# Kernel optimization log

Hardware: AMD Instinct MI355X
Metric: run time of the kernel (lower is better)

## Reference

```python
import jax, jax.numpy as jnp
import numpy as np

DIM = 2048
HID = 5632  # multiple_of*ceil((2/3*8192)/256)
CONV = 4
SEQ = 8192


def setup_inputs() -> dict:
    key = jax.random.key(0)
    ks = jax.random.split(key, 6)
    x = jax.random.normal(ks[0], (1, SEQ, DIM), dtype=jnp.float32)
    cu_seqlens = jnp.array([0, 2048, 4096, 6144, 8192], dtype=jnp.int32)
    s = DIM ** -0.5
    w_w = jax.random.normal(ks[1], (HID, DIM), dtype=jnp.float32) * s
    wz_w = jax.random.normal(ks[2], (HID, DIM), dtype=jnp.float32) * s
    wh_w = jax.random.normal(ks[3], (HID, DIM), dtype=jnp.float32) * s
    wo_w = jax.random.normal(ks[4], (DIM, HID), dtype=jnp.float32) * (HID ** -0.5)
    conv_w = jax.random.normal(ks[5], (HID, CONV), dtype=jnp.float32) * (CONV ** -0.5)
    return {"x": x, "cu_seqlens": cu_seqlens, "w_w": w_w, "wz_w": wz_w,
            "wh_w": wh_w, "wo_w": wo_w, "conv_w": conv_w}


def _segment_ids(cu_seqlens, seq_len):
    start = jnp.zeros((seq_len,), dtype=jnp.int32).at[cu_seqlens[:-1]].set(1)
    return start, jnp.cumsum(start)  # start marker, segment id per position


def _causal_conv(z, conv_w, seg_id):
    # z: (b, s, H); depthwise causal conv, w[:, -1] multiplies current step,
    # masked so taps never cross cu_seqlens boundaries.
    s = z.shape[1]
    out = z * conv_w[:, CONV - 1][None, None, :]
    for k in range(1, CONV):
        zs = jnp.pad(z, ((0, 0), (k, 0), (0, 0)))[:, :s]
        sid = jnp.pad(seg_id, (k, 0))[:s]
        valid = (sid == seg_id) & (jnp.arange(s) >= k)
        out = out + zs * conv_w[:, CONV - 1 - k][None, None, :] * valid[None, :, None].astype(z.dtype)
    return out


def _linear_scan(a, b):
    # h_t = a_t * h_{t-1} + b_t along axis=1, via parallel associative scan
    def combine(l, r):
        al, bl = l
        ar, br = r
        return ar * al, ar * bl + br
    _, h = jax.lax.associative_scan(combine, (a, b), axis=1)
    return h


def reference(x, cu_seqlens, w_w, wz_w, wh_w, wo_w, conv_w):
    bsz, seq_len, _ = x.shape
    w0 = jnp.einsum('bsd,hd->bsh', x, w_w)
    z = jnp.einsum('bsd,hd->bsh', x, wz_w)
    tilde_h = jnp.einsum('bsd,hd->bsh', x, wh_w)
    start, seg_id = _segment_ids(cu_seqlens, seq_len)
    z = jax.nn.sigmoid(_causal_conv(z, conv_w, seg_id))
    a = (1.0 - z) * (1 - start)[None, :, None].astype(z.dtype)  # reset state at seq starts
    b = z * tilde_h
    h = _linear_scan(a, b)
    h = h * jax.nn.silu(w0)
    return jnp.einsum('bsh,dh->bsd', h, wo_w)
```

## Files before the change

### kernel.cpp

```cpp
#include <hip/hip_runtime.h>
#include <stdint.h>

#define DIM 2048
#define HID 5632
#define SEQ 8192
#define NW3 (3*HID)
#define CONV 4
#define CHUNK 64

typedef __attribute__((ext_vector_type(8))) __bf16 bf16x8;
typedef __attribute__((ext_vector_type(4))) float f32x4;
typedef __attribute__((ext_vector_type(4))) uint16_t u16x4;

__device__ __forceinline__ uint16_t f2bf(float f) {
  union { float f; uint32_t u; } v; v.f = f;
  return (uint16_t)((v.u + 0x7FFFu + ((v.u >> 16) & 1u)) >> 16);
}
__device__ __forceinline__ float bf2f(uint16_t h) {
  union { uint32_t u; float f; } v; v.u = ((uint32_t)h) << 16;
  return v.f;
}

__global__ void cvt4_kernel(const float* __restrict__ src, uint16_t* __restrict__ dst, int n4) {
  int i = blockIdx.x * blockDim.x + threadIdx.x;
  if (i >= n4) return;
  float4 v = ((const float4*)src)[i];
  ushort4 o;
  o.x = f2bf(v.x); o.y = f2bf(v.y); o.z = f2bf(v.z); o.w = f2bf(v.w);
  ((ushort4*)dst)[i] = o;
}

__device__ __forceinline__ void load_lds16(const void* g, void* l) {
  __builtin_amdgcn_global_load_lds(
      (__attribute__((address_space(1))) void*)g,
      (__attribute__((address_space(3))) void*)l, 16, 0, 0);
}

template<int LDA, int LDB, int LDC, int KLEN, int OUT_MODE>
__global__ __launch_bounds__(512, 2)
void gemm256(const uint16_t* __restrict__ A, const uint16_t* __restrict__ B,
             void* __restrict__ C, int nbx)
{
  __shared__ alignas(16) uint16_t As[2][2][256][32];
  __shared__ alignas(16) uint16_t Bs[2][2][256][32];
  constexpr int NT = KLEN / 64;

  const int tid  = threadIdx.x;
  const int wave = tid >> 6;
  const int lane = tid & 63;

  const int nwg = (int)gridDim.x;
  const int bid = (int)blockIdx.x;
  const int qq  = nwg >> 3, rr = nwg & 7;
  const int xcd = bid & 7, loc = bid >> 3;
  const int swz = (xcd < rr ? xcd*(qq+1) : rr*(qq+1) + (xcd-rr)*qq) + loc;
  const int row0 = (swz % nbx) * 256;
  const int col0 = (swz / nbx) * 256;

  const uint16_t* Ab = A + (size_t)blockIdx.y * KLEN;
  const uint16_t* Bb = B + (size_t)blockIdx.y * KLEN;

  const int wr = wave >> 2;
  const int wc = wave & 3;
  const int rm = lane & 15;
  const int kq8 = ((lane >> 4) ^ ((rm >> 1) & 3)) * 8;
  const int ri = wr*128 + rm;
  const int ci = wc*64 + rm;

  size_t offA0, offA1, offB0, offB1;
  {
    const int g0 = tid,       r0_ = g0 >> 2, k0_ = (g0 & 3) ^ ((r0_ >> 1) & 3);
    const int g1 = 512 + tid, r1_ = g1 >> 2, k1_ = (g1 & 3) ^ ((r1_ >> 1) & 3);
    offA0 = (size_t)(row0 + r0_)*LDA + k0_*8;
    offA1 = (size_t)(row0 + r1_)*LDA + k1_*8;
    offB0 = (size_t)(col0 + r0_)*LDB + k0_*8;
    offB1 = (size_t)(col0 + r1_)*LDB + k1_*8;
  }

#define STAGE_A(kt,h,buf) do {                                              \
    const size_t ko_ = (size_t)(kt)*64 + (size_t)(h)*32;                    \
    load_lds16(Ab + offA0 + ko_, &As[(buf)][(h)][wave*16][0]);              \
    load_lds16(Ab + offA1 + ko_, &As[(buf)][(h)][128 + wave*16][0]);        \
  } while (0)
#define STAGE_B(kt,h,buf) do {                                              \
    const size_t ko_ = (size_t)(kt)*64 + (size_t)(h)*32;                    \
    load_lds16(Bb + offB0 + ko_, &Bs[(buf)][(h)][wave*16][0]);              \
    load_lds16(Bb + offB1 + ko_, &Bs[(buf)][(h)][128 + wave*16][0]);        \
  } while (0)
#define PIN() __builtin_amdgcn_sched_barrier(0)

  f32x4 acc[8][4];
  #pragma unroll
  for (int i = 0; i < 8; ++i)
    #pragma unroll
    for (int j = 0; j < 4; ++j) acc[i][j] = (f32x4){0.f,0.f,0.f,0.f};

  STAGE_A(0,0,0); STAGE_B(0,0,0);
  STAGE_A(0,1,0); STAGE_B(0,1,0);
  {
    const int t1 = (NT > 1) ? 1 : 0;
    STAGE_A(t1,0,1); STAGE_B(t1,0,1);
  }
  asm volatile("s_waitcnt vmcnt(8)" ::: "memory");
  __builtin_amdgcn_s_barrier();
  PIN();

  #pragma unroll 1
  for (int t = 0; t < NT; ++t) {
    const int c   = t & 1;
    const int tn1 = (t+1 < NT) ? t+1 : NT-1;
    const int tn2 = (t+2 < NT) ? t+2 : NT-1;
    bf16x8 af[4], bfr[4];

    #pragma unroll
    for (int i = 0; i < 4; ++i) af[i]  = *(const bf16x8*)&As[c][0][ri + i*16][kq8];
    #pragma unroll
    for (int j = 0; j < 4; ++j) bfr[j] = *(const bf16x8*)&Bs[c][0][ci + j*16][kq8];
    STAGE_A(tn1, 1, c^1);
    PIN();
    __builtin_amdgcn_s_barrier();
    asm volatile("s_waitcnt lgkmcnt(0)" ::: "memory");
    PIN();
    __builtin_amdgcn_s_setprio(1);
    #pragma unroll
    for (int i = 0; i < 4; ++i)
      #pragma unroll
      for (int j = 0; j < 4; ++j)
        acc[i][j] = __builtin_amdgcn_mfma_f32_16x16x32_bf16(af[i], bfr[j], acc[i][j], 0, 0, 0);
    __builtin_amdgcn_s_setprio(0);
    __builtin_amdgcn_s_barrier();
    PIN();

    #pragma unroll
    for (int i = 0; i < 4; ++i) af[i] = *(const bf16x8*)&As[c][0][ri + (i+4)*16][kq8];
    STAGE_B(tn1, 1, c^1);
    PIN();
    __builtin_amdgcn_s_barrier();
    asm volatile("s_waitcnt lgkmcnt(0)" ::: "memory");
    PIN();
    __builtin_amdgcn_s_setprio(1);
    #pragma unroll
    for (int i = 0; i < 4; ++i)
      #pragma unroll
      for (int j = 0; j < 4; ++j)
        acc[i+4][j] = __builtin_amdgcn_mfma_f32_16x16x32_bf16(af[i], bfr[j], acc[i+4][j], 0, 0, 0);
    __builtin_amdgcn_s_setprio(0);
    asm volatile("s_waitcnt vmcnt(8)" ::: "memory");
    __builtin_amdgcn_s_barrier();
    PIN();

    #pragma unroll
    for (int i = 0; i < 4; ++i) af[i]  = *(const bf16x8*)&As[c][1][ri + i*16][kq8];
    #pragma unroll
    for (int j = 0; j < 4; ++j) bfr[j] = *(const bf16x8*)&Bs[c][1][ci + j*16][kq8];
    STAGE_A(tn2, 0, c);
    PIN();
    __builtin_amdgcn_s_barrier();
    asm volatile("s_waitcnt lgkmcnt(0)" ::: "memory");
    PIN();
    __builtin_amdgcn_s_setprio(1);
    #pragma unroll
    for (int i = 0; i < 4; ++i)
      #pragma unroll
      for (int j = 0; j < 4; ++j)
        acc[i][j] = __builtin_amdgcn_mfma_f32_16x16x32_bf16(af[i], bfr[j], acc[i][j], 0, 0, 0);
    __builtin_amdgcn_s_setprio(0);
    __builtin_amdgcn_s_barrier();
    PIN();

    #pragma unroll
    for (int i = 0; i < 4; ++i) af[i] = *(const bf16x8*)&As[c][1][ri + (i+4)*16][kq8];
    STAGE_B(tn2, 0, c);
    PIN();
    __builtin_amdgcn_s_barrier();
    asm volatile("s_waitcnt lgkmcnt(0)" ::: "memory");
    PIN();
    __builtin_amdgcn_s_setprio(1);
    #pragma unroll
    for (int i = 0; i < 4; ++i)
      #pragma unroll
      for (int j = 0; j < 4; ++j)
        acc[i+4][j] = __builtin_amdgcn_mfma_f32_16x16x32_bf16(af[i], bfr[j], acc[i+4][j], 0, 0, 0);
    __builtin_amdgcn_s_setprio(0);
    asm volatile("s_waitcnt vmcnt(8)" ::: "memory");
    __builtin_amdgcn_s_barrier();
    PIN();
  }
#undef STAGE_A
#undef STAGE_B
#undef PIN

  const int cr = (lane >> 4) * 4;
  const int cc = lane & 15;
  #pragma unroll
  for (int i = 0; i < 8; ++i)
    #pragma unroll
    for (int j = 0; j < 4; ++j) {
      const int r_ = row0 + wr*128 + i*16 + cr;
      const int c_ = col0 + wc*64  + j*16 + cc;
      #pragma unroll
      for (int r = 0; r < 4; ++r) {
        const float v = acc[i][j][r];
        const size_t idx = (size_t)(r_ + r)*LDC + c_;
        if (OUT_MODE == 1)      ((uint16_t*)C)[idx] = f2bf(v);
        else if (OUT_MODE == 2) atomicAdd((float*)C + idx, v);
        else                    ((float*)C)[idx] = v;
      }
    }
}


__device__ __forceinline__ void seg_info(const int* cuv, int ns, int t, int& ss, bool& st) {
  ss = 0; st = false;
  for (int i=0;i<ns;i++) { int cv = cuv[i]; if (cv<=t && cv>ss) ss=cv; if (cv==t) st=true; }
}

__global__ void scan_chunk(const uint16_t* __restrict__ G, int qstart,
                           const uint16_t* __restrict__ zprev,
                           const float* __restrict__ convw,
                           const int* __restrict__ cu, int ncu,
                           float* __restrict__ Ach, float* __restrict__ Bch)
{
  const int h0 = (blockIdx.x * blockDim.x + threadIdx.x) * 4;
  const int c  = blockIdx.y;
  const uint16_t* Z  = G + HID;
  const uint16_t* TH = G + 2*HID;
  float4 wv[4];
  #pragma unroll
  for (int j=0;j<4;j++) wv[j] = ((const float4*)convw)[h0+j];
  int cuv[8];
  int ns = ncu - 1; if (ns > 8) ns = 8;
  for (int i=0;i<ns;i++) cuv[i] = cu[i];
  const int r0 = c * CHUNK;
  const int t0 = qstart + r0;
  float z1[4], z2[4], z3[4];
  if (c == 0) {
    u16x4 a1 = *(const u16x4*)&zprev[2*HID + h0];
    u16x4 a2 = *(const u16x4*)&zprev[1*HID + h0];
    u16x4 a3 = *(const u16x4*)&zprev[0*HID + h0];
    #pragma unroll
    for (int j=0;j<4;j++) {
      z1[j] = (t0-1 >= 0) ? bf2f(a1[j]) : 0.f;
      z2[j] = (t0-2 >= 0) ? bf2f(a2[j]) : 0.f;
      z3[j] = (t0-3 >= 0) ? bf2f(a3[j]) : 0.f;
    }
  } else {
    u16x4 a1 = *(const u16x4*)&Z[(size_t)(r0-1)*NW3 + h0];
    u16x4 a2 = *(const u16x4*)&Z[(size_t)(r0-2)*NW3 + h0];
    u16x4 a3 = *(const u16x4*)&Z[(size_t)(r0-3)*NW3 + h0];
    #pragma unroll
    for (int j=0;j<4;j++) { z1[j]=bf2f(a1[j]); z2[j]=bf2f(a2[j]); z3[j]=bf2f(a3[j]); }
  }
  float Aacc[4] = {1.f,1.f,1.f,1.f};
  float Bacc[4] = {0.f,0.f,0.f,0.f};
  u16x4 zv = *(const u16x4*)&Z[(size_t)r0*NW3 + h0];
  u16x4 tv = *(const u16x4*)&TH[(size_t)r0*NW3 + h0];
  for (int r = r0; r < r0 + CHUNK; ++r) {
    const int rn = (r+1 < r0+CHUNK) ? r+1 : r;
    u16x4 zn = *(const u16x4*)&Z[(size_t)rn*NW3 + h0];
    u16x4 tn = *(const u16x4*)&TH[(size_t)rn*NW3 + h0];
    const int t = qstart + r;
    int ss; bool st;
    seg_info(cuv, ns, t, ss, st);
    const bool k1 = (t-1 >= ss), k2 = (t-2 >= ss), k3 = (t-3 >= ss);
    #pragma unroll
    for (int j=0;j<4;j++) {
      const float zc0 = bf2f(zv[j]);
      float s = zc0*wv[j].w;
      if (k1) s += z1[j]*wv[j].z;
      if (k2) s += z2[j]*wv[j].y;
      if (k3) s += z3[j]*wv[j].x;
      const float zc = 1.f/(1.f + __expf(-s));
      const float a = st ? 0.f : (1.f - zc);
      const float b = zc * bf2f(tv[j]);
      Aacc[j] *= a;
      Bacc[j] = a*Bacc[j] + b;
      z3[j] = z2[j]; z2[j] = z1[j]; z1[j] = zc0;
    }
    zv = zn; tv = tn;
  }
  *(float4*)&Ach[(size_t)c*HID + h0] = make_float4(Aacc[0],Aacc[1],Aacc[2],Aacc[3]);
  *(float4*)&Bch[(size_t)c*HID + h0] = make_float4(Bacc[0],Bacc[1],Bacc[2],Bacc[3]);
}

__global__ void scan_combine(float* __restrict__ Ach, const float* __restrict__ Bch,
                             float* __restrict__ Sc, int first, int nchunk)
{
  const int h0 = (blockIdx.x * blockDim.x + threadIdx.x) * 4;
  float4 s;
  if (first) s = make_float4(0.f,0.f,0.f,0.f);
  else       s = *(const float4*)&Sc[h0];
  for (int c = 0; c < nchunk; ++c) {
    const size_t idx = (size_t)c*HID + h0;
    float4 a = *(const float4*)&Ach[idx];
    float4 b = *(const float4*)&Bch[idx];
    *(float4*)&Ach[idx] = s;
    s.x = a.x*s.x + b.x;
    s.y = a.y*s.y + b.y;
    s.z = a.z*s.z + b.z;
    s.w = a.w*s.w + b.w;
  }
  *(float4*)&Sc[h0] = s;
}

__global__ void scan_final(uint16_t* __restrict__ G, int qstart,
                           const uint16_t* __restrict__ zprev,
                           const float* __restrict__ convw,
                           const int* __restrict__ cu, int ncu,
                           const float* __restrict__ Hin)
{
  const int h0 = (blockIdx.x * blockDim.x + threadIdx.x) * 4;
  const int c  = blockIdx.y;
  const uint16_t* W0 = G;
  const uint16_t* Z  = G + HID;
  uint16_t*       TH = G + 2*HID;
  float4 wv[4];
  #pragma unroll
  for (int j=0;j<4;j++) wv[j] = ((const float4*)convw)[h0+j];
  int cuv[8];
  int ns = ncu - 1; if (ns > 8) ns = 8;
  for (int i=0;i<ns;i++) cuv[i] = cu[i];
  const int r0 = c * CHUNK;
  const int t0 = qstart + r0;
  float z1[4], z2[4], z3[4];
  if (c == 0) {
    u16x4 a1 = *(const u16x4*)&zprev[2*HID + h0];
    u16x4 a2 = *(const u16x4*)&zprev[1*HID + h0];
    u16x4 a3 = *(const u16x4*)&zprev[0*HID + h0];
    #pragma unroll
    for (int j=0;j<4;j++) {
      z1[j] = (t0-1 >= 0) ? bf2f(a1[j]) : 0.f;
      z2[j] = (t0-2 >= 0) ? bf2f(a2[j]) : 0.f;
      z3[j] = (t0-3 >= 0) ? bf2f(a3[j]) : 0.f;
    }
  } else {
    u16x4 a1 = *(const u16x4*)&Z[(size_t)(r0-1)*NW3 + h0];
    u16x4 a2 = *(const u16x4*)&Z[(size_t)(r0-2)*NW3 + h0];
    u16x4 a3 = *(const u16x4*)&Z[(size_t)(r0-3)*NW3 + h0];
    #pragma unroll
    for (int j=0;j<4;j++) { z1[j]=bf2f(a1[j]); z2[j]=bf2f(a2[j]); z3[j]=bf2f(a3[j]); }
  }
  float state[4];
  {
    float4 hv = *(const float4*)&Hin[(size_t)c*HID + h0];
    state[0]=hv.x; state[1]=hv.y; state[2]=hv.z; state[3]=hv.w;
  }
  u16x4 zv = *(const u16x4*)&Z[(size_t)r0*NW3 + h0];
  u16x4 tv = *(const u16x4*)&TH[(size_t)r0*NW3 + h0];
  u16x4 wvv = *(const u16x4*)&W0[(size_t)r0*NW3 + h0];
  for (int r = r0; r < r0 + CHUNK; ++r) {
    const int rn = (r+1 < r0+CHUNK) ? r+1 : r;
    u16x4 zn = *(const u16x4*)&Z[(size_t)rn*NW3 + h0];
    u16x4 tn = *(const u16x4*)&TH[(size_t)rn*NW3 + h0];
    u16x4 wn = *(const u16x4*)&W0[(size_t)rn*NW3 + h0];
    const int t = qstart + r;
    int ss; bool st;
    seg_info(cuv, ns, t, ss, st);
    const bool k1 = (t-1 >= ss), k2 = (t-2 >= ss), k3 = (t-3 >= ss);
    u16x4 outv;
    #pragma unroll
    for (int j=0;j<4;j++) {
      const float zc0 = bf2f(zv[j]);
      float s = zc0*wv[j].w;
      if (k1) s += z1[j]*wv[j].z;
      if (k2) s += z2[j]*wv[j].y;
      if (k3) s += z3[j]*wv[j].x;
      const float zc = 1.f/(1.f + __expf(-s));
      const float a = st ? 0.f : (1.f - zc);
      const float b = zc * bf2f(tv[j]);
      state[j] = a*state[j] + b;
      const float w0v = bf2f(wvv[j]);
      const float silu = w0v / (1.f + __expf(-w0v));
      outv[j] = f2bf(state[j] * silu);
      z3[j] = z2[j]; z2[j] = z1[j]; z1[j] = zc0;
    }
    *(u16x4*)&TH[(size_t)r*NW3 + h0] = outv;
    zv = zn; tv = tn; wvv = wn;
  }
}

__global__ void save_ztail(const uint16_t* __restrict__ G, uint16_t* __restrict__ zprev, int qrows) {
  int i4 = (blockIdx.x * blockDim.x + threadIdx.x) * 4;
  if (i4 >= 3*HID) return;
  int j = i4 / HID;
  int h = i4 - j*HID;
  *(u16x4*)&zprev[i4] = *(const u16x4*)&G[(size_t)(qrows-3+j)*NW3 + HID + h];
}

extern "C" void kernel_launch(void* const* d_in, const int* in_sizes, int n_in,
                              void* d_out, int out_size, void* d_ws, size_t ws_size,
                              hipStream_t stream) {
  const float* x     = (const float*)d_in[0];
  const int*   cu    = (const int*)d_in[1];
  const float* w_w   = (const float*)d_in[2];
  const float* wz_w  = (const float*)d_in[3];
  const float* wh_w  = (const float*)d_in[4];
  const float* wo_w  = (const float*)d_in[5];
  const float* convw = (const float*)d_in[6];
  const int ncu = in_sizes[1];
  float* out = (float*)d_out;

  const size_t base = 92331008ull;
  int qrows = 2048;
  if (ws_size >= base + 8192ull*38592ull) qrows = 8192;
  else if (ws_size >= base + 4096ull*38592ull) qrows = 4096;
  const int nq = SEQ / qrows;
  const int nchunk = qrows / CHUNK;

  char* p = (char*)d_ws;
  uint16_t* w3b  = (uint16_t*)p; p += (size_t)NW3*DIM*2;
  uint16_t* wob  = (uint16_t*)p; p += (size_t)DIM*HID*2;
  float*    Sc   = (float*)p;    p += (size_t)HID*4;
  uint16_t* zprev= (uint16_t*)p; p += (size_t)3*HID*2;
  uint16_t* xseg = (uint16_t*)p; p += (size_t)qrows*DIM*2;
  uint16_t* G    = (uint16_t*)p; p += (size_t)qrows*NW3*2;
  float*    Ach  = (float*)p;    p += (size_t)nchunk*HID*4;
  float*    Bch  = (float*)p;    p += (size_t)nchunk*HID*4;

  {
    int n4 = HID*DIM/4;
    cvt4_kernel<<<(n4+255)/256, 256, 0, stream>>>(w_w,  w3b, n4);
    cvt4_kernel<<<(n4+255)/256, 256, 0, stream>>>(wz_w, w3b + (size_t)HID*DIM, n4);
    cvt4_kernel<<<(n4+255)/256, 256, 0, stream>>>(wh_w, w3b + (size_t)2*HID*DIM, n4);
    n4 = DIM*HID/4;
    cvt4_kernel<<<(n4+255)/256, 256, 0, stream>>>(wo_w, wob, n4);
  }

  if (qrows < 8192)
    hipMemsetAsync(out, 0, (size_t)out_size * sizeof(float), stream);

  for (int s = 0; s < nq; ++s) {
    const int qstart = s * qrows;

    int n4 = qrows*DIM/4;
    cvt4_kernel<<<(n4+255)/256, 256, 0, stream>>>(x + (size_t)qstart*DIM, xseg, n4);

    {
      const int nbx = qrows / 256;
      gemm256<DIM, DIM, NW3, DIM, 1><<<dim3(nbx * (NW3/256), 1), 512, 0, stream>>>(
          xseg, w3b, G, nbx);
    }

    scan_chunk  <<<dim3(11, nchunk), 128, 0, stream>>>(G, qstart, zprev, convw, cu, ncu, Ach, Bch);
    scan_combine<<<11, 128, 0, stream>>>(Ach, Bch, Sc, s == 0 ? 1 : 0, nchunk);
    scan_final  <<<dim3(11, nchunk), 128, 0, stream>>>(G, qstart, zprev, convw, cu, ncu, Ach);

    if (s + 1 < nq)
      save_ztail<<<(3*HID/4+127)/128, 128, 0, stream>>>(G, zprev, qrows);

    if (qrows == 8192) {
      gemm256<NW3, HID, DIM, HID, 0><<<dim3(32*(DIM/256), 1), 512, 0, stream>>>(
          G + 2*HID, wob, out + (size_t)qstart*DIM, 32);
    } else if (qrows == 4096) {
      gemm256<NW3, HID, DIM, HID/2, 2><<<dim3(16*(DIM/256), 2), 512, 0, stream>>>(
          G + 2*HID, wob, out + (size_t)qstart*DIM, 16);
    } else {
      gemm256<NW3, HID, DIM, HID/4, 2><<<dim3(8*(DIM/256), 4), 512, 0, stream>>>(
          G + 2*HID, wob, out + (size_t)qstart*DIM, 8);
    }
  }
}
```

Baseline: 1.557 ms.

## Switch GEMMs to 128x256 tiles with triple-buffered K=32 pipeline and split-K partials

Replaces the 256x256 GEMM tile with a 128x256 tile that uses a three-stage LDS ring and K-steps of 32. This cuts LDS per block so four blocks can be resident per CU, and it drops one barrier per step. The split-K output GEMM no longer uses atomics on a zeroed output. The first K-half now writes into a scratch buffer that aliases the dead G region, the other half writes to out, and an add kernel sums them. The costs are lower data reuse per tile, a narrower pipeline, and an extra elementwise pass over the output.

New measurement: 1.385 ms. 11.0% less time.

```diff
diff --git a/kernel.cpp b/kernel.cpp
--- a/kernel.cpp
+++ b/kernel.cpp
@@ -7,6 +7,7 @@
 #define NW3 (3*HID)
 #define CONV 4
 #define CHUNK 64
+#define PLDC 8448
 
 typedef __attribute__((ext_vector_type(8))) __bf16 bf16x8;
 typedef __attribute__((ext_vector_type(4))) float f32x4;
@@ -36,14 +37,14 @@
       (__attribute__((address_space(3))) void*)l, 16, 0, 0);
 }
 
-template<int LDA, int LDB, int LDC, int KLEN, int OUT_MODE>
-__global__ __launch_bounds__(512, 2)
-void gemm256(const uint16_t* __restrict__ A, const uint16_t* __restrict__ B,
-             void* __restrict__ C, int nbx)
+template<int LDA, int LDB, int LDC, int LDC2, int KLEN, int OUT_MODE>
+__global__ __launch_bounds__(512, 4)
+void gemm128(const uint16_t* __restrict__ A, const uint16_t* __restrict__ B,
+             void* __restrict__ C, float* __restrict__ C2, int nbx)
 {
-  __shared__ alignas(16) uint16_t As[2][2][256][32];
-  __shared__ alignas(16) uint16_t Bs[2][2][256][32];
-  constexpr int NT = KLEN / 64;
+  __shared__ alignas(16) uint16_t As[3][128][32];
+  __shared__ alignas(16) uint16_t Bs[3][256][32];
+  constexpr int NT = KLEN / 32;
 
   const int tid  = threadIdx.x;
   const int wave = tid >> 6;
@@ -54,71 +55,66 @@
   const int qq  = nwg >> 3, rr = nwg & 7;
   const int xcd = bid & 7, loc = bid >> 3;
   const int swz = (xcd < rr ? xcd*(qq+1) : rr*(qq+1) + (xcd-rr)*qq) + loc;
-  const int row0 = (swz % nbx) * 256;
+  const int row0 = (swz % nbx) * 128;
   const int col0 = (swz / nbx) * 256;
 
-  const uint16_t* Ab = A + (size_t)blockIdx.y * KLEN;
-  const uint16_t* Bb = B + (size_t)blockIdx.y * KLEN;
+  const uint16_t* Ab = A + (size_t)blockIdx.z * KLEN;
+  const uint16_t* Bb = B + (size_t)blockIdx.z * KLEN;
 
   const int wr = wave >> 2;
   const int wc = wave & 3;
   const int rm = lane & 15;
   const int kq8 = ((lane >> 4) ^ ((rm >> 1) & 3)) * 8;
-  const int ri = wr*128 + rm;
+  const int ri = wr*64 + rm;
   const int ci = wc*64 + rm;
 
-  size_t offA0, offA1, offB0, offB1;
+  size_t offA, offB0, offB1;
   {
-    const int g0 = tid,       r0_ = g0 >> 2, k0_ = (g0 & 3) ^ ((r0_ >> 1) & 3);
-    const int g1 = 512 + tid, r1_ = g1 >> 2, k1_ = (g1 & 3) ^ ((r1_ >> 1) & 3);
-    offA0 = (size_t)(row0 + r0_)*LDA + k0_*8;
-    offA1 = (size_t)(row0 + r1_)*LDA + k1_*8;
-    offB0 = (size_t)(col0 + r0_)*LDB + k0_*8;
-    offB1 = (size_t)(col0 + r1_)*LDB + k1_*8;
-  }
-
-#define STAGE_A(kt,h,buf) do {                                              \
-    const size_t ko_ = (size_t)(kt)*64 + (size_t)(h)*32;                    \
-    load_lds16(Ab + offA0 + ko_, &As[(buf)][(h)][wave*16][0]);              \
-    load_lds16(Ab + offA1 + ko_, &As[(buf)][(h)][128 + wave*16][0]);        \
-  } while (0)
-#define STAGE_B(kt,h,buf) do {                                              \
-    const size_t ko_ = (size_t)(kt)*64 + (size_t)(h)*32;                    \
-    load_lds16(Bb + offB0 + ko_, &Bs[(buf)][(h)][wave*16][0]);              \
-    load_lds16(Bb + offB1 + ko_, &Bs[(buf)][(h)][128 + wave*16][0]);        \
+    const int ra = tid >> 2,        ka = (tid & 3) ^ ((ra >> 1) & 3);
+    const int rb0 = tid >> 2,       kb0 = (tid & 3) ^ ((rb0 >> 1) & 3);
+    const int g1 = 512 + tid;
+    const int rb1 = g1 >> 2,        kb1 = (g1 & 3) ^ ((rb1 >> 1) & 3);
+    offA  = (size_t)(row0 + ra)*LDA + ka*8;
+    offB0 = (size_t)(col0 + rb0)*LDB + kb0*8;
+    offB1 = (size_t)(col0 + rb1)*LDB + kb1*8;
+  }
+
+#define STAGE(kt,buf) do {                                                  \
+    const size_t ko_ = (size_t)(kt)*32;                                     \
+    load_lds16(Ab + offA  + ko_, &As[(buf)][wave*16][0]);                   \
+    load_lds16(Bb + offB0 + ko_, &Bs[(buf)][wave*16][0]);                   \
+    load_lds16(Bb + offB1 + ko_, &Bs[(buf)][128 + wave*16][0]);             \
   } while (0)
 #define PIN() __builtin_amdgcn_sched_barrier(0)
 
-  f32x4 acc[8][4];
+  f32x4 acc[4][4];
   #pragma unroll
-  for (int i = 0; i < 8; ++i)
+  for (int i = 0; i < 4; ++i)
     #pragma unroll
     for (int j = 0; j < 4; ++j) acc[i][j] = (f32x4){0.f,0.f,0.f,0.f};
 
-  STAGE_A(0,0,0); STAGE_B(0,0,0);
-  STAGE_A(0,1,0); STAGE_B(0,1,0);
+  STAGE(0, 0);
   {
     const int t1 = (NT > 1) ? 1 : 0;
-    STAGE_A(t1,0,1); STAGE_B(t1,0,1);
-  }
-  asm volatile("s_waitcnt vmcnt(8)" ::: "memory");
+    STAGE(t1, 1);
+  }
+  asm volatile("s_waitcnt vmcnt(3)" ::: "memory");
   __builtin_amdgcn_s_barrier();
   PIN();
 
+  int c = 0;
   #pragma unroll 1
   for (int t = 0; t < NT; ++t) {
-    const int c   = t & 1;
-    const int tn1 = (t+1 < NT) ? t+1 : NT-1;
     const int tn2 = (t+2 < NT) ? t+2 : NT-1;
+    int cs = c + 2; if (cs >= 3) cs -= 3;
+
     bf16x8 af[4], bfr[4];
-
-    #pragma unroll
-    for (int i = 0; i < 4; ++i) af[i]  = *(const bf16x8*)&As[c][0][ri + i*16][kq8];
-    #pragma unroll
-    for (int j = 0; j < 4; ++j) bfr[j] = *(const bf16x8*)&Bs[c][0][ci + j*16][kq8];
-    STAGE_A(tn1, 1, c^1);
+    #pragma unroll
+    for (int i = 0; i < 4; ++i) af[i]  = *(const bf16x8*)&As[c][ri + i*16][kq8];
+    #pragma unroll
+    for (int j = 0; j < 4; ++j) bfr[j] = *(const bf16x8*)&Bs[c][ci + j*16][kq8];
+    STAGE(tn2, cs);
     PIN();
-    __builtin_amdgcn_s_barrier();
     asm volatile("s_waitcnt lgkmcnt(0)" ::: "memory");
     PIN();
     __builtin_amdgcn_s_setprio(1);
@@ -128,85 +124,47 @@
       for (int j = 0; j < 4; ++j)
         acc[i][j] = __builtin_amdgcn_mfma_f32_16x16x32_bf16(af[i], bfr[j], acc[i][j], 0, 0, 0);
     __builtin_amdgcn_s_setprio(0);
+    asm volatile("s_waitcnt vmcnt(3)" ::: "memory");
     __builtin_amdgcn_s_barrier();
     PIN();
 
-    #pragma unroll
-    for (int i = 0; i < 4; ++i) af[i] = *(const bf16x8*)&As[c][0][ri + (i+4)*16][kq8];
-    STAGE_B(tn1, 1, c^1);
-    PIN();
-    __builtin_amdgcn_s_barrier();
-    asm volatile("s_waitcnt lgkmcnt(0)" ::: "memory");
-    PIN();
-    __builtin_amdgcn_s_setprio(1);
-    #pragma unroll
-    for (int i = 0; i < 4; ++i)
-      #pragma unroll
-      for (int j = 0; j < 4; ++j)
-        acc[i+4][j] = __builtin_amdgcn_mfma_f32_16x16x32_bf16(af[i], bfr[j], acc[i+4][j], 0, 0, 0);
-    __builtin_amdgcn_s_setprio(0);
-    asm volatile("s_waitcnt vmcnt(8)" ::: "memory");
-    __builtin_amdgcn_s_barrier();
-    PIN();
-
-    #pragma unroll
-    for (int i = 0; i < 4; ++i) af[i]  = *(const bf16x8*)&As[c][1][ri + i*16][kq8];
-    #pragma unroll
-    for (int j = 0; j < 4; ++j) bfr[j] = *(const bf16x8*)&Bs[c][1][ci + j*16][kq8];
-    STAGE_A(tn2, 0, c);
-    PIN();
-    __builtin_amdgcn_s_barrier();
-    asm volatile("s_waitcnt lgkmcnt(0)" ::: "memory");
-    PIN();
-    __builtin_amdgcn_s_setprio(1);
-    #pragma unroll
-    for (int i = 0; i < 4; ++i)
-      #pragma unroll
-      for (int j = 0; j < 4; ++j)
-        acc[i][j] = __builtin_amdgcn_mfma_f32_16x16x32_bf16(af[i], bfr[j], acc[i][j], 0, 0, 0);
-    __builtin_amdgcn_s_setprio(0);
-    __builtin_amdgcn_s_barrier();
-    PIN();
-
-    #pragma unroll
-    for (int i = 0; i < 4; ++i) af[i] = *(const bf16x8*)&As[c][1][ri + (i+4)*16][kq8];
-    STAGE_B(tn2, 0, c);
-    PIN();
-    __builtin_amdgcn_s_barrier();
-    asm volatile("s_waitcnt lgkmcnt(0)" ::: "memory");
-    PIN();
-    __builtin_amdgcn_s_setprio(1);
-    #pragma unroll
-    for (int i = 0; i < 4; ++i)
-      #pragma unroll
-      for (int j = 0; j < 4; ++j)
-        acc[i+4][j] = __builtin_amdgcn_mfma_f32_16x16x32_bf16(af[i], bfr[j], acc[i+4][j], 0, 0, 0);
-    __builtin_amdgcn_s_setprio(0);
-    asm volatile("s_waitcnt vmcnt(8)" ::: "memory");
-    __builtin_amdgcn_s_barrier();
-    PIN();
-  }
-#undef STAGE_A
-#undef STAGE_B
+    c += 1; if (c >= 3) c = 0;
+  }
+#undef STAGE
 #undef PIN
 
   const int cr = (lane >> 4) * 4;
   const int cc = lane & 15;
   #pragma unroll
-  for (int i = 0; i < 8; ++i)
+  for (int i = 0; i < 4; ++i)
     #pragma unroll
     for (int j = 0; j < 4; ++j) {
-      const int r_ = row0 + wr*128 + i*16 + cr;
-      const int c_ = col0 + wc*64  + j*16 + cc;
+      const int r_ = row0 + wr*64 + i*16 + cr;
+      const int c_ = col0 + wc*64 + j*16 + cc;
       #pragma unroll
       for (int r = 0; r < 4; ++r) {
         const float v = acc[i][j][r];
-        const size_t idx = (size_t)(r_ + r)*LDC + c_;
-        if (OUT_MODE == 1)      ((uint16_t*)C)[idx] = f2bf(v);
-        else if (OUT_MODE == 2) atomicAdd((float*)C + idx, v);
-        else                    ((float*)C)[idx] = v;
+        if (OUT_MODE == 1) {
+          ((uint16_t*)C)[(size_t)(r_ + r)*LDC + c_] = f2bf(v);
+        } else if (OUT_MODE == 2) {
+          if (blockIdx.z == 0) C2[(size_t)(r_ + r)*LDC2 + c_] = v;
+          else                 ((float*)C)[(size_t)(r_ + r)*LDC + c_] = v;
+        } else {
+          ((float*)C)[(size_t)(r_ + r)*LDC + c_] = v;
+        }
       }
     }
+}
+
+__global__ void addP_kernel(float* __restrict__ out, const float* __restrict__ P, int n4) {
+  int i = blockIdx.x * blockDim.x + threadIdx.x;
+  if (i >= n4) return;
+  int r  = i >> 9;
+  int c4 = i & 511;
+  float4 a = ((float4*)out)[i];
+  float4 b = *(const float4*)&P[(size_t)r*PLDC + c4*4];
+  a.x += b.x; a.y += b.y; a.z += b.z; a.w += b.w;
+  ((float4*)out)[i] = a;
 }
 
 
@@ -426,9 +384,6 @@
     cvt4_kernel<<<(n4+255)/256, 256, 0, stream>>>(wo_w, wob, n4);
   }
 
-  if (qrows < 8192)
-    hipMemsetAsync(out, 0, (size_t)out_size * sizeof(float), stream);
-
   for (int s = 0; s < nq; ++s) {
     const int qstart = s * qrows;
 
@@ -436,9 +391,9 @@
     cvt4_kernel<<<(n4+255)/256, 256, 0, stream>>>(x + (size_t)qstart*DIM, xseg, n4);
 
     {
-      const int nbx = qrows / 256;
-      gemm256<DIM, DIM, NW3, DIM, 1><<<dim3(nbx * (NW3/256), 1), 512, 0, stream>>>(
-          xseg, w3b, G, nbx);
+      const int nbx = qrows / 128;
+      gemm128<DIM, DIM, NW3, 0, DIM, 1><<<dim3(nbx * (NW3/256), 1, 1), 512, 0, stream>>>(
+          xseg, w3b, G, nullptr, nbx);
     }
 
     scan_chunk  <<<dim3(11, nchunk), 128, 0, stream>>>(G, qstart, zprev, convw, cu, ncu, Ach, Bch);
@@ -448,15 +403,16 @@
     if (s + 1 < nq)
       save_ztail<<<(3*HID/4+127)/128, 128, 0, stream>>>(G, zprev, qrows);
 
+    const int nbx2 = qrows / 128;
+    float* P = (float*)G;
     if (qrows == 8192) {
-      gemm256<NW3, HID, DIM, HID, 0><<<dim3(32*(DIM/256), 1), 512, 0, stream>>>(
-          G + 2*HID, wob, out + (size_t)qstart*DIM, 32);
-    } else if (qrows == 4096) {
-      gemm256<NW3, HID, DIM, HID/2, 2><<<dim3(16*(DIM/256), 2), 512, 0, stream>>>(
-          G + 2*HID, wob, out + (size_t)qstart*DIM, 16);
+      gemm128<NW3, HID, DIM, 0, HID, 0><<<dim3(nbx2*(DIM/256), 1, 1), 512, 0, stream>>>(
+          G + 2*HID, wob, out + (size_t)qstart*DIM, nullptr, nbx2);
     } else {
-      gemm256<NW3, HID, DIM, HID/4, 2><<<dim3(8*(DIM/256), 4), 512, 0, stream>>>(
-          G + 2*HID, wob, out + (size_t)qstart*DIM, 8);
-    }
-  }
-}
+      gemm128<NW3, HID, DIM, PLDC, HID/2, 2><<<dim3(nbx2*(DIM/256), 1, 2), 512, 0, stream>>>(
+          G + 2*HID, wob, out + (size_t)qstart*DIM, P, nbx2);
+      int na = qrows * (DIM/4);
+      addP_kernel<<<(na+255)/256, 256, 0, stream>>>(out + (size_t)qstart*DIM, P, na);
+    }
+  }
+}
```
